# Optimization experiments

Hardware: AMD Instinct MI355X
Metric: run time of the kernel (lower is better)

## Reference

```python
import jax, jax.numpy as jnp
import numpy as np

NUM_HEADS = 16
HEAD_DIM = 64
BATCH = 4
SEQ = 1024
MAX_SEQ_LEN = 2048


def _shift(pos_score):
    # Transformer-XL relative shift. pos_score: (NH, S, S_kv)
    NH, S, S_kv = pos_score.shape
    zero_pad = jnp.zeros((NH, S, 1), dtype=pos_score.dtype)
    padded = jnp.concatenate([zero_pad, pos_score], axis=-1)  # (NH, S, S_kv+1)
    padded = padded.reshape(NH, S_kv + 1, S)
    return padded[:, 1:, :].reshape(NH, S, S_kv)


def setup_inputs() -> dict:
    key = jax.random.key(0)
    ks = jax.random.split(key, 6)
    NH = BATCH * NUM_HEADS
    return {
        "queries": jax.random.normal(ks[0], (NH, SEQ, HEAD_DIM), dtype=jnp.float32),
        "keys": jax.random.normal(ks[1], (NH, SEQ, HEAD_DIM), dtype=jnp.float32),
        "values": jax.random.normal(ks[2], (NH, SEQ, HEAD_DIM), dtype=jnp.float32),
        "u_bias": jax.random.normal(ks[3], (1, NUM_HEADS, 1, HEAD_DIM), dtype=jnp.float32),
        "v_bias": jax.random.normal(ks[4], (1, NUM_HEADS, 1, HEAD_DIM), dtype=jnp.float32),
        "R": jax.random.normal(ks[5], (NUM_HEADS, MAX_SEQ_LEN, HEAD_DIM), dtype=jnp.float32),
    }


def reference(queries, keys, values, u_bias, v_bias, R):
    NH, S, d = queries.shape
    S_kv = keys.shape[1]
    batch = NH // NUM_HEADS

    q = queries * (d ** -0.5)
    q = q.reshape(batch, NUM_HEADS, S, d)
    q_u = (q + u_bias).reshape(NH, S, d)
    q_v = (q + v_bias).reshape(NH, S, d)

    # relative position embeddings, tiled over batch: (NH, S_kv, d)
    R_s = jnp.tile(R[:, :S_kv, :], (batch, 1, 1))

    content_score = jnp.einsum('nsd,ntd->nst', q_u, keys)   # (NH, S, S_kv)
    pos_score = jnp.einsum('nsd,ntd->nst', q_v, R_s)        # (NH, S, S_kv)
    pos_score = _shift(pos_score)

    attn_weights = jax.nn.softmax(content_score + pos_score, axis=-1)
    attn = jnp.einsum('nst,ntd->nsd', attn_weights, values)  # (NH, S, d)
    return attn
```

## Files before the change

kernel.cpp:

```cpp
#include <hip/hip_runtime.h>


#define SQ    1024
#define HD    64
#define NHD   16
#define RMAX  2048

typedef _Float16 f16x8 __attribute__((ext_vector_type(8)));
typedef _Float16 f16x4 __attribute__((ext_vector_type(4)));
typedef short    b16x8 __attribute__((ext_vector_type(8)));
typedef float    f32x4 __attribute__((ext_vector_type(4)));

#define MFMA_F16(A,B,C)  __builtin_amdgcn_mfma_f32_16x16x32_f16((A),(B),(C),0,0,0)
#define MFMA_BF16(A,B,C) __builtin_amdgcn_mfma_f32_16x16x32_bf16((A),(B),(C),0,0,0)

#define L2E    1.44269504088896f
#define NSHIFT (-57.7078016f)

#define KH_OFF   0
#define VT_OFF   (8u << 20)
#define R16_OFF  (18u << 20)
#define WS_NEED  (20u << 20)

__device__ __forceinline__ float exp2fast(float x) {
#if __has_builtin(__builtin_amdgcn_exp2f)
  return __builtin_amdgcn_exp2f(x);
#else
  return __expf(x * 0.693147180559945f);
#endif
}

__device__ __forceinline__ short f2b(float f) {
  unsigned u = __builtin_bit_cast(unsigned, f);
  u += 0x7FFFu + ((u >> 16) & 1u);
  return (short)(u >> 16);
}
__device__ __forceinline__ unsigned pkh(float a, float b) {
  _Float16 h0 = (_Float16)a, h1 = (_Float16)b;
  return (unsigned)__builtin_bit_cast(unsigned short, h0)
       | ((unsigned)__builtin_bit_cast(unsigned short, h1) << 16);
}
__device__ __forceinline__ unsigned pkb2(float a, float b) {
  unsigned ua = __builtin_bit_cast(unsigned, a) + 0x8000u;
  unsigned ub = __builtin_bit_cast(unsigned, b) + 0x8000u;
  return (ub & 0xFFFF0000u) | (ua >> 16);
}
__device__ __forceinline__ int swz(int row, int col) {
  return row*64 + ((((col >> 3) ^ row) & 7) << 3) + (col & 7);
}


__global__ __launch_bounds__(256) void preprep(
    const float* __restrict__ K, const float* __restrict__ R,
    const float* __restrict__ V,
    _Float16* __restrict__ Kh, _Float16* __restrict__ R16,
    short* __restrict__ Vt)
{
  __shared__ float t[64][65];
  const int bid = blockIdx.x, tid = threadIdx.x;
  if (bid < 1024) {
    const int n = bid >> 4, st = bid & 15;
    {
      const int row = tid >> 2, c0 = (tid & 3) * 16;
      const float* src = V + ((size_t)n * SQ + st * 64 + row) * HD + c0;
#pragma unroll
      for (int i = 0; i < 4; ++i) {
        float4 x = ((const float4*)src)[i];
        t[row][c0 + 4*i + 0] = x.x; t[row][c0 + 4*i + 1] = x.y;
        t[row][c0 + 4*i + 2] = x.z; t[row][c0 + 4*i + 3] = x.w;
      }
    }
    __syncthreads();
    {
      const int d = tid >> 2, s0 = (tid & 3) * 16;
      short* dst = Vt + ((size_t)n * 80 + d) * SQ + st * 64 + s0;
#pragma unroll
      for (int i = 0; i < 8; ++i)
        *(unsigned*)(dst + 2*i) = pkb2(t[s0 + 2*i][d], t[s0 + 2*i + 1][d]);
    }
    if (tid < 64) {
      const int s = st * 64 + tid;
      Vt[((size_t)n * 80 + 64) * SQ + s] = (short)0x3F80;
#pragma unroll
      for (int r = 65; r < 80; ++r) Vt[((size_t)n * 80 + r) * SQ + s] = 0;
    }
  } else {
    const int idx = (bid - 1024) * 256 + tid;
    const int nk4 = (64 * SQ * HD) / 4;
    if (idx < nk4) {
      float4 v = ((const float4*)K)[idx];
      f16x4 o = { (_Float16)v.x, (_Float16)v.y, (_Float16)v.z, (_Float16)v.w };
      *(f16x4*)(Kh + 4 * (size_t)idx) = o;
    } else {
      int rr = idx - nk4;
      int h  = rr >> 14, off = rr & 16383;
      float4 v = ((const float4*)R)[((size_t)h << 15) + off];
      f16x4 o = { (_Float16)v.x, (_Float16)v.y, (_Float16)v.z, (_Float16)v.w };
      *(f16x4*)(R16 + 4 * (((size_t)h << 14) + off)) = o;
    }
  }
}


__global__ __launch_bounds__(256, 4) void relpos_sdpa_r11(
    const float* __restrict__ Q, const _Float16* __restrict__ Kh,
    const short* __restrict__ Vtg, const _Float16* __restrict__ R16,
    const float* __restrict__ Ub, const float* __restrict__ Vb,
    float* __restrict__ O)
{
  const int n    = blockIdx.x;
  const int h    = n & (NHD - 1);
  const int a0   = blockIdx.y * 64;
  const int tid  = threadIdx.x;
  const int lane = tid & 63, wave = tid >> 6;
  const int l15  = lane & 15, quad = lane >> 4;

  const float*    Qn  = Q   + (size_t)n * SQ * HD;
  const _Float16* Khn = Kh  + (size_t)n * SQ * HD;
  const short*    Vgn = Vtg + (size_t)n * 80 * SQ;
  const _Float16* Rh  = R16 + (size_t)h * SQ * HD;

  __shared__ __align__(16) char lds[42128];
  _Float16*       Kb   = (_Float16*)lds;
  short*          Vt   = (short*)(lds + 8192);
  unsigned short* Ps   = (unsigned short*)(lds + 16512);
  unsigned*       Pb2  = (unsigned*)(lds + 24704);
  const _Float16* Pb2h = (const _Float16*)Pb2;

  f16x8 quF[2], qvF[5][2];
#pragma unroll
  for (int ks = 0; ks < 2; ++ks) {
    const int db = ks * 32 + quad * 8;
    float ub[8], vb[8];
#pragma unroll
    for (int j = 0; j < 8; ++j) {
      ub[j] = Ub[h*HD + db + j] * L2E;
      vb[j] = Vb[h*HD + db + j] * L2E;
    }
    {
      const float* p = Qn + (size_t)(a0 + 16*wave + l15) * HD + db;
      float4 x0 = ((const float4*)p)[0], x1 = ((const float4*)p)[1];
      f16x8 f;
#pragma unroll
      for (int t = 0; t < 4; ++t) {
        f[t]   = (_Float16)((&x0.x)[t] * (0.125f * L2E) + ub[t]);
        f[t+4] = (_Float16)((&x1.x)[t] * (0.125f * L2E) + ub[t+4]);
      }
      quF[ks] = f;
    }
#pragma unroll
    for (int rt = 0; rt < 5; ++rt) {
      int row = a0 + 16*rt + l15; if (row > SQ-1) row = SQ-1;
      const float* p = Qn + (size_t)row * HD + db;
      float4 x0 = ((const float4*)p)[0], x1 = ((const float4*)p)[1];
      f16x8 f;
#pragma unroll
      for (int t = 0; t < 4; ++t) {
        f[t]   = (_Float16)((&x0.x)[t] * (0.125f * L2E) + vb[t]);
        f[t+4] = (_Float16)((&x1.x)[t] * (0.125f * L2E) + vb[t+4]);
      }
      qvF[rt][ks] = f;
    }
  }

  if (tid < 64) Vt[swz(64, tid)] = (short)0x3F80;

  f32x4 Oacc[5];
#pragma unroll
  for (int ct = 0; ct < 5; ++ct) Oacc[ct] = (f32x4){0.f, 0.f, 0.f, 0.f};

  unsigned ringW[9];
  int ringSlot;
  auto band = [&](int jstart) {
    const int c    = jstart + 16*wave + l15;
    const int j    = (c + 2048) & (SQ - 1);
    ringSlot       = (c + 2048) & 127;
    const _Float16* rp = Rh + (size_t)j * HD + quad * 8;
    f16x8 B0 = *(const f16x8*)rp;
    f16x8 B1 = *(const f16x8*)(rp + 32);
#pragma unroll
    for (int rt = 0; rt < 5; ++rt) {
      f32x4 acc = (f32x4){0.f, 0.f, 0.f, 0.f};
      acc = MFMA_F16(qvF[rt][0], B0, acc);
      acc = MFMA_F16(qvF[rt][1], B1, acc);
      if (rt < 4) {
        ringW[2*rt]     = pkh(acc[0], acc[1]);
        ringW[2*rt + 1] = pkh(acc[2], acc[3]);
      } else {
        ringW[8] = pkh(acc[0], acc[1]);
      }
    }
  };
  auto ringFlush = [&]() {
#pragma unroll
    for (int rt = 0; rt < 4; ++rt) {
      const int rp0 = 8*rt + 2*quad;
      Pb2[rp0*132 + ringSlot]       = ringW[2*rt];
      Pb2[(rp0 + 1)*132 + ringSlot] = ringW[2*rt + 1];
    }
    if (quad == 0) Pb2[32*132 + ringSlot] = ringW[8];
  };

  band(-a0 - 65);  ringFlush();
  band(-a0 - 1);   ringFlush();

  f16x8 kPre[2]; b16x8 vPre[2];
  auto stageLoad = [&](int k0) {
    const _Float16* ks = Khn + (size_t)(k0 + lane) * HD + wave*8;
    kPre[0] = *(const f16x8*)ks;
    kPre[1] = *(const f16x8*)(ks + 32);
    const short* vs = Vgn + (size_t)lane * SQ + k0 + wave*8;
    vPre[0] = *(const b16x8*)vs;
    vPre[1] = *(const b16x8*)(vs + 32);
  };
  auto stageWrite = [&]() {
    *(f16x8*)&Kb[swz(lane, wave*8)]      = kPre[0];
    *(f16x8*)&Kb[swz(lane, 32 + wave*8)] = kPre[1];
    *(b16x8*)&Vt[swz(lane, wave*8)]      = vPre[0];
    *(b16x8*)&Vt[swz(lane, 32 + wave*8)] = vPre[1];
  };

  stageLoad(0);

  const int iiB = 16*wave + 4*quad;

  for (int k0 = 0; k0 < SQ; k0 += 64) {
    __syncthreads();

    stageWrite();
    if (k0 > 0) ringFlush();

    __syncthreads();

    if (k0 < SQ - 64) stageLoad(k0 + 64);

    f32x4 sc[4];
#pragma unroll
    for (int ct = 0; ct < 4; ++ct) {
      f16x8 b0 = *(const f16x8*)&Kb[swz(16*ct + l15, quad*8)];
      f16x8 b1 = *(const f16x8*)&Kb[swz(16*ct + l15, 32 + quad*8)];
      f32x4 acc = (f32x4){NSHIFT, NSHIFT, NSHIFT, NSHIFT};
      acc = MFMA_F16(quF[0], b0, acc);
      acc = MFMA_F16(quF[1], b1, acc);
      sc[ct] = acc;
    }

    const int dlt = k0 - a0;
    if (dlt == 0 || dlt == 64) {
#pragma unroll
      for (int r = 0; r < 4; ++r) {
        const int ii = iiB + r;
        const int adA = (ii >> 1) * 264 + (ii & 1);
        const int adB = ((ii + 1) >> 1) * 264 + ((ii + 1) & 1);
#pragma unroll
        for (int ct = 0; ct < 4; ++ct) {
          const int e    = dlt + 16*ct + l15 - ii;
          const int u    = (e > 0) ? 1 : 0;
          const int slot = (e - 1 - u) & 127;
          float pos = (float)Pb2h[(u ? adB : adA) + 2*slot];
          float s   = sc[ct][r] + ((e == 1) ? 0.f : pos);
          sc[ct][r] = exp2fast(s);
        }
      }
    } else {
      const int uu    = (dlt > 0) ? 1 : 0;
      const int cbase = dlt - 1 - uu + l15 - iiB + 2048;
#pragma unroll
      for (int r = 0; r < 4; ++r) {
        const int iu = iiB + r + uu;
        const int ad = (iu >> 1) * 264 + (iu & 1);
        const int c0 = cbase - r;
#pragma unroll
        for (int ct = 0; ct < 4; ++ct) {
          const int slot = (c0 + 16*ct) & 127;
          float pos = (float)Pb2h[ad + 2*slot];
          sc[ct][r] = exp2fast(sc[ct][r] + pos);
        }
      }
    }

#pragma unroll
    for (int r = 0; r < 4; ++r) {
      unsigned w0 = pkb2(sc[0][r], sc[1][r]);
      unsigned w1 = pkb2(sc[2][r], sc[3][r]);
      const int row = iiB + r;
      Ps[swz(row, l15)]      = (unsigned short)w0;
      Ps[swz(row, 16 + l15)] = (unsigned short)(w0 >> 16);
      Ps[swz(row, 32 + l15)] = (unsigned short)w1;
      Ps[swz(row, 48 + l15)] = (unsigned short)(w1 >> 16);
    }

    b16x8 pA0 = *(const b16x8*)&Ps[swz(16*wave + l15, quad*8)];
    b16x8 pA1 = *(const b16x8*)&Ps[swz(16*wave + l15, 32 + quad*8)];
#pragma unroll
    for (int ct = 0; ct < 5; ++ct) {
      b16x8 v0 = *(const b16x8*)&Vt[swz(16*ct + l15, quad*8)];
      b16x8 v1 = *(const b16x8*)&Vt[swz(16*ct + l15, 32 + quad*8)];
      Oacc[ct] = MFMA_BF16(pA0, v0, Oacc[ct]);
      Oacc[ct] = MFMA_BF16(pA1, v1, Oacc[ct]);
    }

    if (k0 < SQ - 64) band(k0 + 64 - a0 - 1);
  }

#pragma unroll
  for (int r = 0; r < 4; ++r) {
    float l   = __shfl(Oacc[4][r], lane & 48);
    float inv = 1.0f / l;
    const size_t rowo = (size_t)n * SQ * HD + (size_t)(a0 + iiB + r) * HD;
#pragma unroll
    for (int ct = 0; ct < 4; ++ct)
      O[rowo + 16*ct + l15] = Oacc[ct][r] * inv;
  }
}


__global__ __launch_bounds__(256, 4) void relpos_sdpa_fb(
    const float* __restrict__ Q, const float* __restrict__ K,
    const float* __restrict__ V, const float* __restrict__ Ub,
    const float* __restrict__ Vb, const float* __restrict__ R,
    float* __restrict__ O)
{
  const int n    = blockIdx.x;
  const int h    = n & (NHD - 1);
  const int a0   = blockIdx.y * 64;
  const int tid  = threadIdx.x;
  const int lane = tid & 63, wave = tid >> 6;
  const int l15  = lane & 15, quad = lane >> 4;

  const float* Qn = Q + (size_t)n * SQ * HD;
  const float* Kn = K + (size_t)n * SQ * HD;
  const float* Vn = V + (size_t)n * SQ * HD;
  const float* Rh = R + (size_t)h * RMAX * HD;

  __shared__ __align__(16) char lds[38656];
  _Float16* Kb = (_Float16*)lds;
  short*    Ps = (short*)lds;
  short*    Vt = (short*)(lds + 9216);
  _Float16* Pb = (_Float16*)(lds + 9216 + 11520);

  f16x8 quF[2], qvF[5][2];
#pragma unroll
  for (int ks = 0; ks < 2; ++ks) {
    const int db = ks * 32 + quad * 8;
    float ub[8], vb[8];
#pragma unroll
    for (int j = 0; j < 8; ++j) { ub[j] = Ub[h*HD + db + j]; vb[j] = Vb[h*HD + db + j]; }
    {
      const float* p = Qn + (size_t)(a0 + 16*wave + l15) * HD + db;
      f16x8 f;
#pragma unroll
      for (int j = 0; j < 8; ++j) f[j] = (_Float16)(p[j] * 0.125f + ub[j]);
      quF[ks] = f;
    }
#pragma unroll
    for (int rt = 0; rt < 5; ++rt) {
      int row = a0 + 16*rt + l15; if (row > SQ-1) row = SQ-1;
      const float* p = Qn + (size_t)row * HD + db;
      f16x8 f;
#pragma unroll
      for (int j = 0; j < 8; ++j) f[j] = (_Float16)(p[j] * 0.125f + vb[j]);
      qvF[rt][ks] = f;
    }
  }

  if (tid < 64) Vt[64*72 + tid] = (short)0x3F80;

  f32x4 Oacc[5];
#pragma unroll
  for (int ct = 0; ct < 5; ++ct) Oacc[ct] = (f32x4){0.f, 0.f, 0.f, 0.f};

  auto band = [&](int jstart) {
    const int c    = jstart + 16*wave + l15;
    const int j    = (c + 2048) & (SQ - 1);
    const int slot = (c + 2048) & 127;
    const float* rp = Rh + (size_t)j * HD + quad * 8;
    f16x8 B0, B1;
    {
      float4 x0 = *(const float4*)(rp),      x1 = *(const float4*)(rp + 4);
      float4 y0 = *(const float4*)(rp + 32), y1 = *(const float4*)(rp + 36);
#pragma unroll
      for (int t = 0; t < 4; ++t) { B0[t] = (_Float16)(&x0.x)[t]; B0[t+4] = (_Float16)(&x1.x)[t]; }
#pragma unroll
      for (int t = 0; t < 4; ++t) { B1[t] = (_Float16)(&y0.x)[t]; B1[t+4] = (_Float16)(&y1.x)[t]; }
    }
#pragma unroll
    for (int rt = 0; rt < 5; ++rt) {
      f32x4 acc = (f32x4){0.f, 0.f, 0.f, 0.f};
      acc = MFMA_F16(qvF[rt][0], B0, acc);
      acc = MFMA_F16(qvF[rt][1], B1, acc);
      const int row = 16*rt + 4*quad;
      if (rt < 4) {
        *(unsigned*)&Pb[slot*70 + row]     = pkh(acc[0], acc[1]);
        *(unsigned*)&Pb[slot*70 + row + 2] = pkh(acc[2], acc[3]);
      } else if (quad == 0) {
        *(unsigned*)&Pb[slot*70 + row]     = pkh(acc[0], acc[1]);
      }
    }
  };

  band(-a0 - 65);
  band(-a0 - 1);

  const int sr = tid >> 2, sc4 = tid & 3;
  const int iiB = 16*wave + 4*quad;

  for (int k0 = 0; k0 < SQ; k0 += 64) {
    __syncthreads();
    {
      const float* src = Kn + (size_t)(k0 + sr) * HD + sc4 * 16;
      float4 x0 = *(const float4*)(src),     x1 = *(const float4*)(src + 4);
      float4 y0 = *(const float4*)(src + 8), y1 = *(const float4*)(src + 12);
      f16x8 lo, hi;
#pragma unroll
      for (int t = 0; t < 4; ++t) { lo[t] = (_Float16)(&x0.x)[t]; lo[t+4] = (_Float16)(&x1.x)[t]; }
#pragma unroll
      for (int t = 0; t < 4; ++t) { hi[t] = (_Float16)(&y0.x)[t]; hi[t+4] = (_Float16)(&y1.x)[t]; }
      *(f16x8*)&Kb[sr*72 + sc4*16]     = lo;
      *(f16x8*)&Kb[sr*72 + sc4*16 + 8] = hi;
    }
    {
      const int g = lane >> 3;
#pragma unroll
      for (int i = 0; i < 8; ++i) {
        int bp = 8*wave + (i ^ g);
        float v0 = Vn[(size_t)(k0 + 2*bp)     * HD + lane];
        float v1 = Vn[(size_t)(k0 + 2*bp + 1) * HD + lane];
        *(unsigned*)&Vt[lane*72 + 2*bp] = pkb2(v0, v1);
      }
    }
    __syncthreads();

    f32x4 sc[4];
#pragma unroll
    for (int ct = 0; ct < 4; ++ct) {
      f16x8 b0 = *(const f16x8*)&Kb[(16*ct + l15)*72 + quad*8];
      f16x8 b1 = *(const f16x8*)&Kb[(16*ct + l15)*72 + 32 + quad*8];
      f32x4 acc = (f32x4){0.f, 0.f, 0.f, 0.f};
      acc = MFMA_F16(quF[0], b0, acc);
      acc = MFMA_F16(quF[1], b1, acc);
      sc[ct] = acc;
    }

    const int dlt = k0 - a0;
#pragma unroll
    for (int r = 0; r < 4; ++r) {
      const int ii = iiB + r;
#pragma unroll
      for (int ct = 0; ct < 4; ++ct) {
        const int e    = dlt + 16*ct + l15 - ii;
        const int u    = (e > 0) ? 1 : 0;
        const int slot = (e - 1 - u + 2048) & 127;
        float pos = (float)Pb[slot*70 + ii + u];
        float s   = sc[ct][r] + ((e == 1) ? 0.f : pos);
        sc[ct][r] = __expf(s - 40.0f);
      }
    }
    __syncthreads();

#pragma unroll
    for (int r = 0; r < 4; ++r)
#pragma unroll
      for (int ct = 0; ct < 4; ++ct)
        Ps[(iiB + r)*68 + 16*ct + l15] = f2b(sc[ct][r]);

    b16x8 pA0 = *(const b16x8*)&Ps[(16*wave + l15)*68 + quad*8];
    b16x8 pA1 = *(const b16x8*)&Ps[(16*wave + l15)*68 + 32 + quad*8];
#pragma unroll
    for (int ct = 0; ct < 5; ++ct) {
      b16x8 v0 = *(const b16x8*)&Vt[(16*ct + l15)*72 + quad*8];
      b16x8 v1 = *(const b16x8*)&Vt[(16*ct + l15)*72 + 32 + quad*8];
      Oacc[ct] = MFMA_BF16(pA0, v0, Oacc[ct]);
      Oacc[ct] = MFMA_BF16(pA1, v1, Oacc[ct]);
    }

    if (k0 < SQ - 64) band(k0 + 64 - a0 - 1);
  }

#pragma unroll
  for (int r = 0; r < 4; ++r) {
    float l   = __shfl(Oacc[4][r], lane & 48);
    float inv = 1.0f / l;
    const size_t rowo = (size_t)n * SQ * HD + (size_t)(a0 + iiB + r) * HD;
#pragma unroll
    for (int ct = 0; ct < 4; ++ct)
      O[rowo + 16*ct + l15] = Oacc[ct][r] * inv;
  }
}

extern "C" void kernel_launch(void* const* d_in, const int* in_sizes, int n_in,
                              void* d_out, int out_size, void* d_ws, size_t ws_size,
                              hipStream_t stream) {
  const float* Q  = (const float*)d_in[0];
  const float* K  = (const float*)d_in[1];
  const float* V  = (const float*)d_in[2];
  const float* Ub = (const float*)d_in[3];
  const float* Vb = (const float*)d_in[4];
  const float* R  = (const float*)d_in[5];
  float* O = (float*)d_out;

  if (ws_size >= WS_NEED) {
    _Float16* Kh  = (_Float16*)((char*)d_ws + KH_OFF);
    short*    Vt  = (short*)((char*)d_ws + VT_OFF);
    _Float16* R16 = (_Float16*)((char*)d_ws + R16_OFF);

    preprep<<<6144, 256, 0, stream>>>(K, R, V, Kh, R16, Vt);

    dim3 grid(64, 16);
    relpos_sdpa_r11<<<grid, 256, 0, stream>>>(Q, Kh, Vt, R16, Ub, Vb, O);
  } else {
    dim3 grid(64, 16);
    relpos_sdpa_fb<<<grid, 256, 0, stream>>>(Q, K, V, Ub, Vb, R, O);
  }
}
```

Before: 177.7 us.

## Keep P in registers by transposing the score MFMA and feeding the PV MFMA directly

Swaps the operand order of the QK^T MFMA so each lane's accumulator layout matches the A-operand layout of a 16x16x16 bf16 MFMA. The probabilities can then go straight from registers into the PV product, removing the LDS write/read round trip for P and the Ps buffer. The softmax denominator now comes from an extra MFMA against a ones vector instead of an appended ones row in V. Launch bounds drop from 4 to 3 blocks per SIMD and LDS shrinks. The trade is more, smaller MFMAs and possibly lower occupancy.

```diff
diff --git a/kernel.cpp b/kernel.cpp
--- a/kernel.cpp
+++ b/kernel.cpp
@@ -9,7 +9,9 @@
 typedef _Float16 f16x8 __attribute__((ext_vector_type(8)));
 typedef _Float16 f16x4 __attribute__((ext_vector_type(4)));
 typedef short    b16x8 __attribute__((ext_vector_type(8)));
+typedef short    b16x4 __attribute__((ext_vector_type(4)));
 typedef float    f32x4 __attribute__((ext_vector_type(4)));
+typedef unsigned u32x2 __attribute__((ext_vector_type(2)));
 
 #define MFMA_F16(A,B,C)  __builtin_amdgcn_mfma_f32_16x16x32_f16((A),(B),(C),0,0,0)
 #define MFMA_BF16(A,B,C) __builtin_amdgcn_mfma_f32_16x16x32_bf16((A),(B),(C),0,0,0)
@@ -27,6 +29,16 @@
   return __builtin_amdgcn_exp2f(x);
 #else
   return __expf(x * 0.693147180559945f);
+#endif
+}
+
+__device__ __forceinline__ f32x4 mfma16bf(b16x4 a, b16x4 b, f32x4 c) {
+#if __has_builtin(__builtin_amdgcn_mfma_f32_16x16x16bf16_1k)
+  return __builtin_amdgcn_mfma_f32_16x16x16bf16_1k(a, b, c, 0, 0, 0);
+#else
+  b16x8 az = {a[0], a[1], a[2], a[3], 0, 0, 0, 0};
+  b16x8 bz = {b[0], b[1], b[2], b[3], 0, 0, 0, 0};
+  return MFMA_BF16(az, bz, c);
 #endif
 }
 
@@ -102,7 +114,7 @@
 }
 
 
-__global__ __launch_bounds__(256, 4) void relpos_sdpa_r11(
+__global__ __launch_bounds__(256, 3) void relpos_sdpa_r14(
     const float* __restrict__ Q, const _Float16* __restrict__ Kh,
     const short* __restrict__ Vtg, const _Float16* __restrict__ R16,
     const float* __restrict__ Ub, const float* __restrict__ Vb,
@@ -120,11 +132,10 @@
   const short*    Vgn = Vtg + (size_t)n * 80 * SQ;
   const _Float16* Rh  = R16 + (size_t)h * SQ * HD;
 
-  __shared__ __align__(16) char lds[42128];
+  __shared__ __align__(16) char lds[33808];
   _Float16*       Kb   = (_Float16*)lds;
   short*          Vt   = (short*)(lds + 8192);
-  unsigned short* Ps   = (unsigned short*)(lds + 16512);
-  unsigned*       Pb2  = (unsigned*)(lds + 24704);
+  unsigned*       Pb2  = (unsigned*)(lds + 16384);
   const _Float16* Pb2h = (const _Float16*)Pb2;
 
   f16x8 quF[2], qvF[5][2];
@@ -163,11 +174,12 @@
     }
   }
 
-  if (tid < 64) Vt[swz(64, tid)] = (short)0x3F80;
-
-  f32x4 Oacc[5];
-#pragma unroll
-  for (int ct = 0; ct < 5; ++ct) Oacc[ct] = (f32x4){0.f, 0.f, 0.f, 0.f};
+  f32x4 Oacc[4], acc_l;
+#pragma unroll
+  for (int ct = 0; ct < 4; ++ct) Oacc[ct] = (f32x4){0.f, 0.f, 0.f, 0.f};
+  acc_l = (f32x4){0.f, 0.f, 0.f, 0.f};
+
+  const b16x4 ONESB = {(short)0x3F80, (short)0x3F80, (short)0x3F80, (short)0x3F80};
 
   unsigned ringW[9];
   int ringSlot;
@@ -223,6 +235,7 @@
   stageLoad(0);
 
   const int iiB = 16*wave + 4*quad;
+  const int iQ  = 16*wave + l15;
 
   for (int k0 = 0; k0 < SQ; k0 += 64) {
     __syncthreads();
@@ -237,24 +250,24 @@
     f32x4 sc[4];
 #pragma unroll
     for (int ct = 0; ct < 4; ++ct) {
-      f16x8 b0 = *(const f16x8*)&Kb[swz(16*ct + l15, quad*8)];
-      f16x8 b1 = *(const f16x8*)&Kb[swz(16*ct + l15, 32 + quad*8)];
+      f16x8 ka = *(const f16x8*)&Kb[swz(16*ct + l15, quad*8)];
+      f16x8 kb = *(const f16x8*)&Kb[swz(16*ct + l15, 32 + quad*8)];
       f32x4 acc = (f32x4){NSHIFT, NSHIFT, NSHIFT, NSHIFT};
-      acc = MFMA_F16(quF[0], b0, acc);
-      acc = MFMA_F16(quF[1], b1, acc);
+      acc = MFMA_F16(ka, quF[0], acc);
+      acc = MFMA_F16(kb, quF[1], acc);
       sc[ct] = acc;
     }
 
-    const int dlt = k0 - a0;
-    if (dlt == 0 || dlt == 64) {
-#pragma unroll
-      for (int r = 0; r < 4; ++r) {
-        const int ii = iiB + r;
-        const int adA = (ii >> 1) * 264 + (ii & 1);
-        const int adB = ((ii + 1) >> 1) * 264 + ((ii + 1) & 1);
-#pragma unroll
-        for (int ct = 0; ct < 4; ++ct) {
-          const int e    = dlt + 16*ct + l15 - ii;
+    const int base = k0 - a0 - 16*wave;
+    if (k0 == a0 || k0 == a0 + 64) {
+      const int adA = (iQ >> 1) * 264 + (iQ & 1);
+      const int adB = ((iQ + 1) >> 1) * 264 + ((iQ + 1) & 1);
+#pragma unroll
+      for (int ct = 0; ct < 4; ++ct) {
+        const int e0 = base + 16*ct + 4*quad - l15;
+#pragma unroll
+        for (int r = 0; r < 4; ++r) {
+          const int e    = e0 + r;
           const int u    = (e > 0) ? 1 : 0;
           const int slot = (e - 1 - u) & 127;
           float pos = (float)Pb2h[(u ? adB : adA) + 2*slot];
@@ -263,16 +276,15 @@
         }
       }
     } else {
-      const int uu    = (dlt > 0) ? 1 : 0;
-      const int cbase = dlt - 1 - uu + l15 - iiB + 2048;
-#pragma unroll
-      for (int r = 0; r < 4; ++r) {
-        const int iu = iiB + r + uu;
-        const int ad = (iu >> 1) * 264 + (iu & 1);
-        const int c0 = cbase - r;
-#pragma unroll
-        for (int ct = 0; ct < 4; ++ct) {
-          const int slot = (c0 + 16*ct) & 127;
+      const int u  = (k0 > a0) ? 1 : 0;
+      const int iu = iQ + u;
+      const int ad = (iu >> 1) * 264 + (iu & 1);
+      const int sb = base - 1 - u + 4*quad - l15 + 2048;
+#pragma unroll
+      for (int ct = 0; ct < 4; ++ct) {
+#pragma unroll
+        for (int r = 0; r < 4; ++r) {
+          const int slot = (sb + 16*ct + r) & 127;
           float pos = (float)Pb2h[ad + 2*slot];
           sc[ct][r] = exp2fast(sc[ct][r] + pos);
         }
@@ -280,24 +292,16 @@
     }
 
 #pragma unroll
-    for (int r = 0; r < 4; ++r) {
-      unsigned w0 = pkb2(sc[0][r], sc[1][r]);
-      unsigned w1 = pkb2(sc[2][r], sc[3][r]);
-      const int row = iiB + r;
-      Ps[swz(row, l15)]      = (unsigned short)w0;
-      Ps[swz(row, 16 + l15)] = (unsigned short)(w0 >> 16);
-      Ps[swz(row, 32 + l15)] = (unsigned short)w1;
-      Ps[swz(row, 48 + l15)] = (unsigned short)(w1 >> 16);
-    }
-
-    b16x8 pA0 = *(const b16x8*)&Ps[swz(16*wave + l15, quad*8)];
-    b16x8 pA1 = *(const b16x8*)&Ps[swz(16*wave + l15, 32 + quad*8)];
-#pragma unroll
-    for (int ct = 0; ct < 5; ++ct) {
-      b16x8 v0 = *(const b16x8*)&Vt[swz(16*ct + l15, quad*8)];
-      b16x8 v1 = *(const b16x8*)&Vt[swz(16*ct + l15, 32 + quad*8)];
-      Oacc[ct] = MFMA_BF16(pA0, v0, Oacc[ct]);
-      Oacc[ct] = MFMA_BF16(pA1, v1, Oacc[ct]);
+    for (int ctk = 0; ctk < 4; ++ctk) {
+      unsigned lo = pkb2(sc[ctk][0], sc[ctk][1]);
+      unsigned hi = pkb2(sc[ctk][2], sc[ctk][3]);
+      b16x4 aF = __builtin_bit_cast(b16x4, (u32x2){lo, hi});
+      acc_l = mfma16bf(aF, ONESB, acc_l);
+#pragma unroll
+      for (int ctd = 0; ctd < 4; ++ctd) {
+        b16x4 bF = *(const b16x4*)&Vt[swz(16*ctd + l15, 16*ctk + 4*quad)];
+        Oacc[ctd] = mfma16bf(aF, bF, Oacc[ctd]);
+      }
     }
 
     if (k0 < SQ - 64) band(k0 + 64 - a0 - 1);
@@ -305,8 +309,7 @@
 
 #pragma unroll
   for (int r = 0; r < 4; ++r) {
-    float l   = __shfl(Oacc[4][r], lane & 48);
-    float inv = 1.0f / l;
+    float inv = 1.0f / acc_l[r];
     const size_t rowo = (size_t)n * SQ * HD + (size_t)(a0 + iiB + r) * HD;
 #pragma unroll
     for (int ct = 0; ct < 4; ++ct)
@@ -507,7 +510,7 @@
     preprep<<<6144, 256, 0, stream>>>(K, R, V, Kh, R16, Vt);
 
     dim3 grid(64, 16);
-    relpos_sdpa_r11<<<grid, 256, 0, stream>>>(Q, Kh, Vt, R16, Ub, Vb, O);
+    relpos_sdpa_r14<<<grid, 256, 0, stream>>>(Q, Kh, Vt, R16, Ub, Vb, O);
   } else {
     dim3 grid(64, 16);
     relpos_sdpa_fb<<<grid, 256, 0, stream>>>(Q, K, V, Ub, Vb, R, O);
```

Result: no change. 175.3 us (-1.4%).
